# Performance work log

Hardware: AMD Instinct MI355X
Metric: run time of the kernel (lower is better)

## Reference

```python
import jax, jax.numpy as jnp
import numpy as np

N_NODES = 100000
N_EDGES = 600000
N_FEAT = 128
DIM = 128
N_LAYERS = 4
N_GRAPHS = 1000
BN_EPS = 1e-4


def setup_inputs() -> dict:
    key = jax.random.key(0)
    ks = jax.random.split(key, 12)
    s = 0.05
    x = jax.random.normal(ks[0], (N_NODES, N_FEAT), dtype=jnp.float32)
    edge_index = jax.random.randint(ks[1], (2, N_EDGES), 0, N_NODES, dtype=jnp.int64)
    batch = jnp.sort(jax.random.randint(ks[2], (N_NODES,), 0, N_GRAPHS, dtype=jnp.int64))
    pre_w = jax.random.normal(ks[3], (N_FEAT, DIM), dtype=jnp.float32) * s
    pre_b = jnp.zeros((DIM,), dtype=jnp.float32)
    # GIN MLP weights (first layer input is DIM since pre projects to DIM)
    conv_w1 = jax.random.normal(ks[4], (N_LAYERS, DIM, DIM), dtype=jnp.float32) * s
    conv_w2 = jax.random.normal(ks[5], (N_LAYERS, DIM, DIM), dtype=jnp.float32) * s
    bn_g = jnp.ones((N_LAYERS, DIM), dtype=jnp.float32)
    bn_b = jnp.zeros((N_LAYERS, DIM), dtype=jnp.float32)
    ed = DIM * N_LAYERS  # embedding_dim = 512
    ff_w1 = jax.random.normal(ks[6], (ed, ed), dtype=jnp.float32) * s
    ff_w2 = jax.random.normal(ks[7], (ed, ed), dtype=jnp.float32) * s
    ff_w3 = jax.random.normal(ks[8], (ed, ed), dtype=jnp.float32) * s
    ff_sc = jax.random.normal(ks[9], (ed, ed), dtype=jnp.float32) * s
    return dict(x=x, edge_index=edge_index, batch=batch, pre_w=pre_w, pre_b=pre_b,
                conv_w1=conv_w1, conv_w2=conv_w2, bn_g=bn_g, bn_b=bn_b,
                ff_w1=ff_w1, ff_w2=ff_w2, ff_w3=ff_w3, ff_sc=ff_sc)


def reference(x, edge_index, batch, pre_w, pre_b, conv_w1, conv_w2, bn_g, bn_b,
              ff_w1, ff_w2, ff_w3, ff_sc):
    lrelu = jax.nn.leaky_relu  # negative_slope=0.01 matches torch default
    n = x.shape[0]
    src, dst = edge_index[0], edge_index[1]

    h = x @ pre_w + pre_b  # [N, DIM]
    xs = []
    for i in range(conv_w1.shape[0]):
        # GINConv (eps=0): nn(x + sum_{j->i} x_j); gather at src, scatter-add at dst
        agg = jax.ops.segment_sum(h[src], dst, num_segments=n)
        h2 = h + agg
        h2 = lrelu(h2 @ conv_w1[i]) @ conv_w2[i]
        # BatchNorm1d (training mode, biased variance, eps=1e-4)
        mean = jnp.mean(h2, axis=0)
        var = jnp.var(h2, axis=0)
        h = (h2 - mean) * jax.lax.rsqrt(var + BN_EPS) * bn_g[i] + bn_b[i]
        xs.append(h)

    # global_add_pool per layer, then concat -> [G, DIM*L]
    pooled = [jax.ops.segment_sum(hl, batch, num_segments=N_GRAPHS) for hl in xs]
    y = jnp.concatenate(pooled, axis=1)

    z = lrelu(lrelu(lrelu(y @ ff_w1) @ ff_w2) @ ff_w3) + y @ ff_sc
    return z
```

## Files before the change

kernel.cpp:

```cpp
#include <hip/hip_runtime.h>
#include <hip/hip_bf16.h>

typedef __hip_bfloat16 bf16;
typedef unsigned int u32;
typedef __attribute__((ext_vector_type(8))) short short8v;
typedef __attribute__((ext_vector_type(4))) float f32x4;

__device__ __forceinline__ float lrelu_f(float v) { return v > 0.f ? v : 0.01f * v; }
__device__ __forceinline__ float bf_lo(u32 u) { return __uint_as_float(u << 16); }
__device__ __forceinline__ float bf_hi(u32 u) { return __uint_as_float(u & 0xffff0000u); }
__device__ __forceinline__ unsigned short bbits(float v) {
    union { bf16 b; unsigned short s; } u; u.b = __float2bfloat16(v); return u.s;
}
__device__ __forceinline__ u32 pack2(float a, float b) {
    return (u32)bbits(a) | ((u32)bbits(b) << 16);
}
__device__ __forceinline__ float ld_ext(const void* p, size_t idx, int f32f) {
    return f32f ? ((const float*)p)[idx] : __bfloat162float(((const bf16*)p)[idx]);
}

__global__ void probe_k(const int* __restrict__ ei, const int* __restrict__ batch,
                        const u32* __restrict__ bng, int nedges, int nnodes,
                        int* __restrict__ flags, float* __restrict__ scaleA,
                        float* __restrict__ shiftA)
{
    __shared__ int nz[2];
    if (threadIdx.x < 2) nz[threadIdx.x] = 0;
    __syncthreads();
    int t = threadIdx.x;
    if (ei[(nedges + 2 * t) | 1] != 0) atomicAdd(&nz[0], 1);
    if (batch[((nnodes >> 1) + 2 * t) | 1] != 0) atomicAdd(&nz[1], 1);
    if (t < 128) { scaleA[t] = 1.f; shiftA[t] = 0.f; }
    __syncthreads();
    if (t == 0) {
        flags[0] = (nz[0] == 0) ? 1 : 0;
        flags[1] = (nz[1] == 0) ? 1 : 0;
        flags[2] = (bng[0] == 0x3F800000u) ? 1 : 0;
    }
}

__global__ __launch_bounds__(256)
void hist_k(const int* __restrict__ ei, int* __restrict__ deg, int nedges,
            const int* __restrict__ flags)
{
    int e = blockIdx.x * 256 + threadIdx.x;
    if (e >= nedges) return;
    int f = flags[0];
    int dst = f ? ei[(nedges + e) << 1] : ei[nedges + e];
    atomicAdd(&deg[dst], 1);
}

__global__ __launch_bounds__(256)
void scan1_k(const int* __restrict__ deg, int* __restrict__ bsum, int n)
{
    __shared__ int l[256];
    int t = threadIdx.x, i = blockIdx.x * 256 + t;
    l[t] = (i < n) ? deg[i] : 0;
    __syncthreads();
    for (int off = 128; off > 0; off >>= 1) {
        if (t < off) l[t] += l[t + off];
        __syncthreads();
    }
    if (t == 0) bsum[blockIdx.x] = l[0];
}
__global__ __launch_bounds__(1024)
void scan2_k(int* __restrict__ bsum, int nb)
{
    __shared__ int l[1024];
    int t = threadIdx.x;
    int orig = (t < nb) ? bsum[t] : 0;
    l[t] = orig;
    __syncthreads();
    for (int off = 1; off < 1024; off <<= 1) {
        int v = (t >= off) ? l[t - off] : 0;
        __syncthreads();
        l[t] += v;
        __syncthreads();
    }
    if (t < nb) bsum[t] = l[t] - orig;
}
__global__ __launch_bounds__(256)
void scan3_k(const int* __restrict__ deg, const int* __restrict__ bsum,
             int* __restrict__ rowptr, int* __restrict__ cursor, int n)
{
    __shared__ int l[256];
    int t = threadIdx.x, i = blockIdx.x * 256 + t;
    int d = (i < n) ? deg[i] : 0;
    l[t] = d;
    __syncthreads();
    for (int off = 1; off < 256; off <<= 1) {
        int v = (t >= off) ? l[t - off] : 0;
        __syncthreads();
        l[t] += v;
        __syncthreads();
    }
    int excl = l[t] - d + bsum[blockIdx.x];
    if (i < n) {
        rowptr[i] = excl;
        cursor[i] = excl;
        if (i == n - 1) rowptr[n] = excl + d;
    }
}

__global__ __launch_bounds__(256)
void fill_k(const int* __restrict__ ei, int* __restrict__ cursor,
            int* __restrict__ srcs, int nedges, const int* __restrict__ flags)
{
    int e = blockIdx.x * 256 + threadIdx.x;
    if (e >= nedges) return;
    int f = flags[0];
    int src = ei[e << f];
    int dst = f ? ei[(nedges + e) << 1] : ei[nedges + e];
    int pos = atomicAdd(&cursor[dst], 1);
    srcs[pos] = src;
}

__global__ __launch_bounds__(256)
void wprep_all_k(const void* __restrict__ pre_w, const void* __restrict__ w1,
                 const void* __restrict__ w2, const void* __restrict__ f0,
                 const void* __restrict__ f1, const void* __restrict__ f2,
                 const void* __restrict__ f3, bf16* __restrict__ Wf,
                 const int* __restrict__ flags)
{
    int e = blockIdx.x * 256 + threadIdx.x;
    if (e >= 1196032) return;
    const void* W; int K, wstride, l, r;
    if (e < 16384)       { W = pre_w; K = 128; wstride = 128; l = 0; r = e; }
    else if (e < 81920)  { int q = e - 16384; W = w1; K = 128; wstride = 128; l = q >> 14; r = q & 16383; }
    else if (e < 147456) { int q = e - 81920; W = w2; K = 128; wstride = 128; l = q >> 14; r = q & 16383; }
    else {
        int q = e - 147456; int m = q >> 18; r = q & 262143;
        W = (m == 0) ? f0 : (m == 1) ? f1 : (m == 2) ? f2 : f3;
        K = 512; wstride = 512; l = 0;
    }
    int KS = K >> 5;
    int j = r & 7, lane = (r >> 3) & 63;
    int rem = r >> 9;
    int ks = rem % KS, nt = rem / KS;
    int k = ks * 32 + ((lane >> 4) << 3) + j;
    int n = nt * 16 + (lane & 15);
    Wf[e] = __float2bfloat16(ld_ext(W, (size_t)(l * K + k) * wstride + n, flags[2]));
}

template<int SRC, int MODE, int OBF>
__global__ __launch_bounds__(256)
void mgemm_k(const void* __restrict__ A, const bf16* __restrict__ Wf,
             const void* __restrict__ bias, void* __restrict__ out,
             int nrows, int K, int astride, int ostride, const int* __restrict__ flags)
{
    const int KS = K >> 5;
    const int t = threadIdx.x, w = t >> 6, lane = t & 63;
    const int quad = lane >> 4, lr = lane & 15;
    const int rbase = blockIdx.x * 64 + w * 16;
    const int arow = min(rbase + lr, nrows - 1);
    const int ntg0 = blockIdx.y * 8;
    const int f32f = flags[2];

    f32x4 acc[8];
    #pragma unroll
    for (int i = 0; i < 8; ++i) acc[i] = (f32x4){0.f, 0.f, 0.f, 0.f};

    for (int ks = 0; ks < KS; ++ks) {
        const int kof = ks * 32 + quad * 8;
        short8v a;
        if (SRC == 0 || f32f) {
            const float* Af = (const float*)A + (size_t)arow * astride + kof;
            float4 p0 = *(const float4*)Af;
            float4 p1 = *(const float4*)(Af + 4);
            a[0] = (short)bbits(p0.x); a[1] = (short)bbits(p0.y);
            a[2] = (short)bbits(p0.z); a[3] = (short)bbits(p0.w);
            a[4] = (short)bbits(p1.x); a[5] = (short)bbits(p1.y);
            a[6] = (short)bbits(p1.z); a[7] = (short)bbits(p1.w);
        } else {
            a = *(const short8v*)((const short*)A + (size_t)arow * astride + kof);
        }
        #pragma unroll
        for (int nt = 0; nt < 8; ++nt) {
            const short8v b = *(const short8v*)&Wf[(((size_t)(ntg0 + nt) * KS + ks) * 64 + lane) * 8];
            acc[nt] = __builtin_amdgcn_mfma_f32_16x16x32_bf16(a, b, acc[nt], 0, 0, 0);
        }
    }

    #pragma unroll
    for (int nt = 0; nt < 8; ++nt) {
        const int col = (ntg0 + nt) * 16 + lr;
        float bv = 0.f;
        if (MODE == 0 && bias != nullptr) bv = ld_ext(bias, col, f32f);
        #pragma unroll
        for (int r = 0; r < 4; ++r) {
            int orow = rbase + quad * 4 + r;
            if (orow < nrows) {
                float v = acc[nt][r] + bv;
                if (MODE == 1) v = lrelu_f(v);
                if (OBF) ((bf16*)out)[(size_t)orow * ostride + col] = __float2bfloat16(v);
                else     ((float*)out)[(size_t)orow * ostride + col] = v;
            }
        }
    }
}

__global__ __launch_bounds__(256, 2)
void conv_k(const u32* __restrict__ aggb, const bf16* __restrict__ Wf1,
            const bf16* __restrict__ Wf2, u32* __restrict__ h2,
            float* __restrict__ psum, float* __restrict__ psq,
            int nrows, int ntiles, int npairs)
{
    __shared__ bf16 PT[2][16][136];
    __shared__ float sblk[128], qblk[128];
    const int t = threadIdx.x, w = t >> 6, lane = t & 63;
    const int quad = lane >> 4, lr = lane & 15;
    const int pair = w >> 1, hw = w & 1;
    const int gpair = blockIdx.x * 2 + pair;
    const int chb = hw * 64;

    short8v w1f[4][4], w2f[4][4];
    #pragma unroll
    for (int i = 0; i < 4; ++i)
        #pragma unroll
        for (int ks = 0; ks < 4; ++ks) {
            int ntb = hw * 4 + i;
            w1f[i][ks] = *(const short8v*)&Wf1[((ntb * 4 + ks) * 64 + lane) * 8];
            w2f[i][ks] = *(const short8v*)&Wf2[((ntb * 4 + ks) * 64 + lane) * 8];
        }

    if (t < 128) { sblk[t] = 0.f; qblk[t] = 0.f; }
    __syncthreads();

    f32x4 s8[4], q8[4];
    #pragma unroll
    for (int i = 0; i < 4; ++i) { s8[i] = (f32x4){0,0,0,0}; q8[i] = (f32x4){0,0,0,0}; }

    const int iters = (ntiles + npairs - 1) / npairs;
    for (int it = 0; it < iters; ++it) {
        const int tile = gpair + it * npairs;
        const bool act = tile < ntiles;
        const int nodeu = act ? tile * 16 + lr : 0;
        const int node = min(nodeu, nrows - 1);
        const bool valid = act && (nodeu < nrows);

        if (act) {
            f32x4 acc[4];
            #pragma unroll
            for (int i = 0; i < 4; ++i) acc[i] = (f32x4){0,0,0,0};
            #pragma unroll
            for (int ks = 0; ks < 4; ++ks) {
                const short8v bfrag = *(const short8v*)&aggb[(size_t)node * 64 + ks * 16 + quad * 4];
                #pragma unroll
                for (int i = 0; i < 4; ++i)
                    acc[i] = __builtin_amdgcn_mfma_f32_16x16x32_bf16(w1f[i][ks], bfrag, acc[i], 0, 0, 0);
            }
            #pragma unroll
            for (int i = 0; i < 4; ++i) {
                u32* dp = (u32*)&PT[pair][lr][chb + i * 16 + quad * 4];
                dp[0] = pack2(lrelu_f(acc[i][0]), lrelu_f(acc[i][1]));
                dp[1] = pack2(lrelu_f(acc[i][2]), lrelu_f(acc[i][3]));
            }
        }
        __syncthreads();
        if (act) {
            f32x4 acc2[4];
            #pragma unroll
            for (int i = 0; i < 4; ++i) acc2[i] = (f32x4){0,0,0,0};
            #pragma unroll
            for (int ks = 0; ks < 4; ++ks) {
                const short8v pfrag = *(const short8v*)&PT[pair][lr][ks * 32 + quad * 8];
                #pragma unroll
                for (int i = 0; i < 4; ++i)
                    acc2[i] = __builtin_amdgcn_mfma_f32_16x16x32_bf16(w2f[i][ks], pfrag, acc2[i], 0, 0, 0);
            }
            if (valid) {
                #pragma unroll
                for (int i = 0; i < 4; ++i) {
                    u32* o = &h2[(size_t)nodeu * 64 + (chb >> 1) + i * 8 + quad * 2];
                    o[0] = pack2(acc2[i][0], acc2[i][1]);
                    o[1] = pack2(acc2[i][2], acc2[i][3]);
                    s8[i] += acc2[i];
                    q8[i] += acc2[i] * acc2[i];
                }
            }
        }
        __syncthreads();
    }

    #pragma unroll
    for (int i = 0; i < 4; ++i)
        #pragma unroll
        for (int r = 0; r < 4; ++r) {
            int ch = chb + i * 16 + quad * 4 + r;
            atomicAdd(&sblk[ch], s8[i][r]);
            atomicAdd(&qblk[ch], q8[i][r]);
        }
    __syncthreads();
    if (t < 128) {
        psum[(size_t)blockIdx.x * 128 + t] = sblk[t];
        psq[(size_t)blockIdx.x * 128 + t] = qblk[t];
    }
}

__global__ __launch_bounds__(256)
void reduce_bn_k(const float* __restrict__ psum, const float* __restrict__ psq,
                 const void* __restrict__ g, const void* __restrict__ b,
                 float* __restrict__ scale, float* __restrict__ shift,
                 float inv_n, int layer, int nblk, const int* __restrict__ flags)
{
    __shared__ float ls[256], lq[256];
    int c = blockIdx.x, t = threadIdx.x;
    float s = 0.f, q = 0.f;
    for (int i = t; i < nblk; i += 256) {
        s += psum[(size_t)i * 128 + c];
        q += psq[(size_t)i * 128 + c];
    }
    ls[t] = s; lq[t] = q;
    __syncthreads();
    for (int off = 128; off > 0; off >>= 1) {
        if (t < off) { ls[t] += ls[t + off]; lq[t] += lq[t + off]; }
        __syncthreads();
    }
    if (t == 0) {
        int f32f = flags[2];
        size_t off = (size_t)layer * 128 + c;
        float mean = ls[0] * inv_n;
        float var = lq[0] * inv_n - mean * mean;
        float sc = ld_ext(g, off, f32f) * rsqrtf(fmaxf(var, 0.f) + 1e-4f);
        scale[c] = sc;
        shift[c] = ld_ext(b, off, f32f) - mean * sc;
    }
}

__global__ __launch_bounds__(256)
void aggregate_k(const int* __restrict__ rowptr, const int* __restrict__ srcs,
                 const u32* __restrict__ h2, u32* __restrict__ aggb,
                 const float* __restrict__ scale, const float* __restrict__ shift, int nnodes)
{
    int node = blockIdx.x * 4 + (threadIdx.x >> 6);
    if (node >= nnodes) return;
    int lane = threadIdx.x & 63;
    u32 u = h2[(size_t)node * 64 + lane];
    float ax = bf_lo(u), ay = bf_hi(u);
    int lo = rowptr[node], hi = rowptr[node + 1];
    int e = lo;
    for (; e + 4 <= hi; e += 4) {
        int s0 = srcs[e], s1 = srcs[e + 1], s2 = srcs[e + 2], s3 = srcs[e + 3];
        u32 v0 = h2[(size_t)s0 * 64 + lane];
        u32 v1 = h2[(size_t)s1 * 64 + lane];
        u32 v2 = h2[(size_t)s2 * 64 + lane];
        u32 v3 = h2[(size_t)s3 * 64 + lane];
        ax += bf_lo(v0) + bf_lo(v1) + bf_lo(v2) + bf_lo(v3);
        ay += bf_hi(v0) + bf_hi(v1) + bf_hi(v2) + bf_hi(v3);
    }
    for (; e < hi; ++e) {
        u32 v = h2[(size_t)srcs[e] * 64 + lane];
        ax += bf_lo(v);
        ay += bf_hi(v);
    }
    float cnt = (float)(hi - lo + 1);
    int c = lane * 2;
    float r0 = fmaf(ax, scale[c], shift[c] * cnt);
    float r1 = fmaf(ay, scale[c + 1], shift[c + 1] * cnt);
    aggb[(size_t)node * 64 + lane] = pack2(r0, r1);
}

__device__ __forceinline__ int lower_bound_b(const int* b, int n, int key, int fb)
{
    int lo = 0, hi = n;
    while (lo < hi) {
        int m = (lo + hi) >> 1;
        if (b[m << fb] < key) lo = m + 1; else hi = m;
    }
    return lo;
}

__global__ __launch_bounds__(256)
void pool_k(const u32* __restrict__ h2, const int* __restrict__ batch,
            float* __restrict__ y, int layer, int nnodes, int ngraphs,
            const float* __restrict__ scale, const float* __restrict__ shift,
            const int* __restrict__ flags)
{
    int g = blockIdx.x * 4 + (threadIdx.x >> 6);
    if (g >= ngraphs) return;
    int t = threadIdx.x & 63;
    int fb = flags[1];
    int lo = lower_bound_b(batch, nnodes, g, fb);
    int hi = lower_bound_b(batch, nnodes, g + 1, fb);
    float s0 = 0.f, s1 = 0.f;
    int i = lo;
    for (; i + 4 <= hi; i += 4) {
        u32 u0 = h2[(size_t)i * 64 + t];
        u32 u1 = h2[(size_t)(i + 1) * 64 + t];
        u32 u2 = h2[(size_t)(i + 2) * 64 + t];
        u32 u3 = h2[(size_t)(i + 3) * 64 + t];
        s0 += bf_lo(u0) + bf_lo(u1) + bf_lo(u2) + bf_lo(u3);
        s1 += bf_hi(u0) + bf_hi(u1) + bf_hi(u2) + bf_hi(u3);
    }
    for (; i < hi; ++i) {
        u32 u = h2[(size_t)i * 64 + t];
        s0 += bf_lo(u);
        s1 += bf_hi(u);
    }
    float cnt = (float)(hi - lo);
    int c = t * 2;
    float* yp = &y[(size_t)g * 512 + layer * 128 + c];
    yp[0] = fmaf(s0, scale[c], shift[c] * cnt);
    yp[1] = fmaf(s1, scale[c + 1], shift[c + 1] * cnt);
}

__global__ __launch_bounds__(256)
void final_k(const float* __restrict__ a, const float* __restrict__ b,
             float* __restrict__ out, int n)
{
    int i = blockIdx.x * 256 + threadIdx.x;
    if (i < n) out[i] = a[i] + b[i];
}

extern "C" void kernel_launch(void* const* d_in, const int* in_sizes, int n_in,
                              void* d_out, int out_size, void* d_ws, size_t ws_size,
                              hipStream_t stream)
{
    const void* x       = d_in[0];
    const int*  ei      = (const int*)d_in[1];
    const int*  batch   = (const int*)d_in[2];
    const void* pre_w   = d_in[3];
    const void* pre_b   = d_in[4];
    const void* conv_w1 = d_in[5];
    const void* conv_w2 = d_in[6];
    const void* bn_g    = d_in[7];
    const void* bn_b    = d_in[8];

    const int n_nodes  = in_sizes[2];
    const int n_edges  = in_sizes[1] / 2;
    const int n_graphs = out_size / 512;
    const size_t nf = (size_t)n_nodes * 128;
    const int nsb = (n_nodes + 255) / 256;
    const int NCONVB = 512;
    const int ntiles = (n_nodes + 15) / 16;
    const int npairs = NCONVB * 2;

    float* ws      = (float*)d_ws;
    int*   flags   = (int*)ws;
    int*   bsum    = (int*)(ws + 16);
    float* scaleA  = ws + 1056;
    float* shiftA  = scaleA + 5 * 128;
    float* psum    = shiftA + 5 * 128;
    float* psq     = psum + (size_t)NCONVB * 128;
    float* y       = psq + (size_t)NCONVB * 128;
    float* tA      = y  + (size_t)n_graphs * 512;
    float* tB      = tA + (size_t)n_graphs * 512;
    u32*   bufA    = (u32*)(tB + (size_t)n_graphs * 512);
    u32*   bufB    = bufA + nf / 2;
    int*   deg     = (int*)(bufB + nf / 2);
    int*   rowptr  = deg + n_nodes;
    int*   srcs    = rowptr + n_nodes + 1;
    bf16*  Wfn     = (bf16*)(((uintptr_t)(srcs + n_edges) + 15) & ~(uintptr_t)15);
    bf16*  Wff     = Wfn + 9 * 16384;

    probe_k<<<1, 256, 0, stream>>>(ei, batch, (const u32*)bn_g, n_edges, n_nodes,
                                   flags, scaleA, shiftA);

    hipMemsetAsync(deg, 0, n_nodes * sizeof(int), stream);
    hist_k<<<(n_edges + 255) / 256, 256, 0, stream>>>(ei, deg, n_edges, flags);
    scan1_k<<<nsb, 256, 0, stream>>>(deg, bsum, n_nodes);
    scan2_k<<<1, 1024, 0, stream>>>(bsum, nsb);
    scan3_k<<<nsb, 256, 0, stream>>>(deg, bsum, rowptr, deg, n_nodes);
    fill_k<<<(n_edges + 255) / 256, 256, 0, stream>>>(ei, deg, srcs, n_edges, flags);

    wprep_all_k<<<(1196032 + 255) / 256, 256, 0, stream>>>(
        pre_w, conv_w1, conv_w2, d_in[9], d_in[10], d_in[11], d_in[12], Wfn, flags);

    const dim3 gpre((n_nodes + 63) / 64, 1);
    const dim3 gf((n_graphs + 63) / 64, 4);

    mgemm_k<1, 0, 1><<<gpre, 256, 0, stream>>>(x, Wfn, pre_b, bufA, n_nodes, 128, 128, 128, flags);

    for (int l = 0; l < 4; ++l) {
        aggregate_k<<<(n_nodes + 3) / 4, 256, 0, stream>>>(
            rowptr, srcs, bufA, bufB, scaleA + l * 128, shiftA + l * 128, n_nodes);
        conv_k<<<NCONVB, 256, 0, stream>>>(bufB, Wfn + (1 + l) * 16384, Wfn + (5 + l) * 16384,
                                           bufA, psum, psq, n_nodes, ntiles, npairs);
        reduce_bn_k<<<128, 256, 0, stream>>>(psum, psq, bn_g, bn_b,
                                             scaleA + (l + 1) * 128, shiftA + (l + 1) * 128,
                                             1.f / (float)n_nodes, l, NCONVB, flags);
        pool_k<<<(n_graphs + 3) / 4, 256, 0, stream>>>(
            bufA, batch, y, l, n_nodes, n_graphs,
            scaleA + (l + 1) * 128, shiftA + (l + 1) * 128, flags);
    }

    mgemm_k<0, 0, 0><<<gf, 256, 0, stream>>>(y,  Wff + 3ull * 262144, nullptr, tB, n_graphs, 512, 512, 512, flags);
    mgemm_k<0, 1, 0><<<gf, 256, 0, stream>>>(y,  Wff + 0ull * 262144, nullptr, tA, n_graphs, 512, 512, 512, flags);
    mgemm_k<0, 1, 0><<<gf, 256, 0, stream>>>(tA, Wff + 1ull * 262144, nullptr, y,  n_graphs, 512, 512, 512, flags);
    mgemm_k<0, 1, 0><<<gf, 256, 0, stream>>>(y,  Wff + 2ull * 262144, nullptr, tA, n_graphs, 512, 512, 512, flags);

    final_k<<<(n_graphs * 512 + 255) / 256, 256, 0, stream>>>(tA, tB, (float*)d_out, n_graphs * 512);
}
```

Before: 811.3 us.

## Add persistent register-weight pre-projection kernel and prefetch conv input tiles

Replaces the generic mgemm pre-projection with a persistent kernel that keeps the weight fragments in registers and converts x to bf16 on the fly. conv_k now prefetches the next tile's aggregated input while computing the current one, and uses wider vector stores. BN partial statistics are now accumulated with per-tile LDS atomics instead of register accumulators flushed once at the end. This frees registers, but the extra LDS atomics in the inner loop add contention.

Measured after the change: 1.381 ms. 1.7x slower.

```diff
diff --git a/kernel.cpp b/kernel.cpp
--- a/kernel.cpp
+++ b/kernel.cpp
@@ -200,6 +200,73 @@
 }
 
 __global__ __launch_bounds__(256, 2)
+void pre_k(const void* __restrict__ x, const bf16* __restrict__ Wf,
+           const void* __restrict__ bias, u32* __restrict__ h,
+           int nrows, int ntiles, int npairs, const int* __restrict__ flags)
+{
+    const int t = threadIdx.x, w = t >> 6, lane = t & 63;
+    const int quad = lane >> 4, lr = lane & 15;
+    const int gpair = blockIdx.x * 2 + (w >> 1);
+    const int hw = w & 1;
+    const int chb = hw * 64;
+    const int f32f = flags[2];
+
+    short8v wf[4][4];
+    #pragma unroll
+    for (int i = 0; i < 4; ++i)
+        #pragma unroll
+        for (int ks = 0; ks < 4; ++ks) {
+            wf[i][ks] = *(const short8v*)&Wf[(((hw * 4 + i) * 4 + ks) * 64 + lane) * 8];
+            asm volatile("" : "+v"(wf[i][ks]));
+        }
+    float bv[4][4];
+    #pragma unroll
+    for (int i = 0; i < 4; ++i)
+        #pragma unroll
+        for (int r = 0; r < 4; ++r)
+            bv[i][r] = ld_ext(bias, chb + i * 16 + quad * 4 + r, f32f);
+
+    const int iters = (ntiles + npairs - 1) / npairs;
+    for (int it = 0; it < iters; ++it) {
+        const int tile = gpair + it * npairs;
+        if (tile >= ntiles) break;
+        const int nodeu = tile * 16 + lr;
+        const int node = min(nodeu, nrows - 1);
+
+        f32x4 acc[4];
+        #pragma unroll
+        for (int i = 0; i < 4; ++i) acc[i] = (f32x4){0,0,0,0};
+        #pragma unroll
+        for (int ks = 0; ks < 4; ++ks) {
+            short8v bfrag;
+            if (f32f) {
+                const float* xp = (const float*)x + (size_t)node * 128 + ks * 32 + quad * 8;
+                float4 p0 = *(const float4*)xp;
+                float4 p1 = *(const float4*)(xp + 4);
+                bfrag[0] = (short)bbits(p0.x); bfrag[1] = (short)bbits(p0.y);
+                bfrag[2] = (short)bbits(p0.z); bfrag[3] = (short)bbits(p0.w);
+                bfrag[4] = (short)bbits(p1.x); bfrag[5] = (short)bbits(p1.y);
+                bfrag[6] = (short)bbits(p1.z); bfrag[7] = (short)bbits(p1.w);
+            } else {
+                bfrag = *(const short8v*)((const short*)x + (size_t)node * 128 + ks * 32 + quad * 8);
+            }
+            #pragma unroll
+            for (int i = 0; i < 4; ++i)
+                acc[i] = __builtin_amdgcn_mfma_f32_16x16x32_bf16(wf[i][ks], bfrag, acc[i], 0, 0, 0);
+        }
+        if (nodeu < nrows) {
+            #pragma unroll
+            for (int i = 0; i < 4; ++i) {
+                uint2 o;
+                o.x = pack2(acc[i][0] + bv[i][0], acc[i][1] + bv[i][1]);
+                o.y = pack2(acc[i][2] + bv[i][2], acc[i][3] + bv[i][3]);
+                *(uint2*)&h[(size_t)nodeu * 64 + (chb >> 1) + i * 8 + quad * 2] = o;
+            }
+        }
+    }
+}
+
+__global__ __launch_bounds__(256, 2)
 void conv_k(const u32* __restrict__ aggb, const bf16* __restrict__ Wf1,
             const bf16* __restrict__ Wf2, u32* __restrict__ h2,
             float* __restrict__ psum, float* __restrict__ psq,
@@ -221,43 +288,55 @@
             int ntb = hw * 4 + i;
             w1f[i][ks] = *(const short8v*)&Wf1[((ntb * 4 + ks) * 64 + lane) * 8];
             w2f[i][ks] = *(const short8v*)&Wf2[((ntb * 4 + ks) * 64 + lane) * 8];
+            asm volatile("" : "+v"(w1f[i][ks]));
+            asm volatile("" : "+v"(w2f[i][ks]));
         }
 
     if (t < 128) { sblk[t] = 0.f; qblk[t] = 0.f; }
     __syncthreads();
 
-    f32x4 s8[4], q8[4];
-    #pragma unroll
-    for (int i = 0; i < 4; ++i) { s8[i] = (f32x4){0,0,0,0}; q8[i] = (f32x4){0,0,0,0}; }
+    int tileC = gpair;
+    bool actC = tileC < ntiles;
+    int nodeuC = tileC * 16 + lr;
+    short8v bcur[4];
+    if (actC) {
+        int nd = min(nodeuC, nrows - 1);
+        #pragma unroll
+        for (int ks = 0; ks < 4; ++ks)
+            bcur[ks] = *(const short8v*)&aggb[(size_t)nd * 64 + ks * 16 + quad * 4];
+    }
 
     const int iters = (ntiles + npairs - 1) / npairs;
     for (int it = 0; it < iters; ++it) {
-        const int tile = gpair + it * npairs;
-        const bool act = tile < ntiles;
-        const int nodeu = act ? tile * 16 + lr : 0;
-        const int node = min(nodeu, nrows - 1);
-        const bool valid = act && (nodeu < nrows);
-
-        if (act) {
+        const int tileN = tileC + npairs;
+        const bool actN = tileN < ntiles;
+        short8v bnxt[4];
+        if (actN) {
+            int ndN = min(tileN * 16 + lr, nrows - 1);
+            #pragma unroll
+            for (int ks = 0; ks < 4; ++ks)
+                bnxt[ks] = *(const short8v*)&aggb[(size_t)ndN * 64 + ks * 16 + quad * 4];
+        }
+
+        if (actC) {
             f32x4 acc[4];
             #pragma unroll
             for (int i = 0; i < 4; ++i) acc[i] = (f32x4){0,0,0,0};
             #pragma unroll
-            for (int ks = 0; ks < 4; ++ks) {
-                const short8v bfrag = *(const short8v*)&aggb[(size_t)node * 64 + ks * 16 + quad * 4];
+            for (int ks = 0; ks < 4; ++ks)
                 #pragma unroll
                 for (int i = 0; i < 4; ++i)
-                    acc[i] = __builtin_amdgcn_mfma_f32_16x16x32_bf16(w1f[i][ks], bfrag, acc[i], 0, 0, 0);
+                    acc[i] = __builtin_amdgcn_mfma_f32_16x16x32_bf16(w1f[i][ks], bcur[ks], acc[i], 0, 0, 0);
+            #pragma unroll
+            for (int i = 0; i < 4; ++i) {
+                uint2 p;
+                p.x = pack2(lrelu_f(acc[i][0]), lrelu_f(acc[i][1]));
+                p.y = pack2(lrelu_f(acc[i][2]), lrelu_f(acc[i][3]));
+                *(uint2*)&PT[pair][lr][chb + i * 16 + quad * 4] = p;
             }
-            #pragma unroll
-            for (int i = 0; i < 4; ++i) {
-                u32* dp = (u32*)&PT[pair][lr][chb + i * 16 + quad * 4];
-                dp[0] = pack2(lrelu_f(acc[i][0]), lrelu_f(acc[i][1]));
-                dp[1] = pack2(lrelu_f(acc[i][2]), lrelu_f(acc[i][3]));
-            }
-        }
-        __syncthreads();
-        if (act) {
+        }
+        __syncthreads();
+        if (actC) {
             f32x4 acc2[4];
             #pragma unroll
             for (int i = 0; i < 4; ++i) acc2[i] = (f32x4){0,0,0,0};
@@ -268,29 +347,28 @@
                 for (int i = 0; i < 4; ++i)
                     acc2[i] = __builtin_amdgcn_mfma_f32_16x16x32_bf16(w2f[i][ks], pfrag, acc2[i], 0, 0, 0);
             }
-            if (valid) {
+            if (nodeuC < nrows) {
                 #pragma unroll
                 for (int i = 0; i < 4; ++i) {
-                    u32* o = &h2[(size_t)nodeu * 64 + (chb >> 1) + i * 8 + quad * 2];
-                    o[0] = pack2(acc2[i][0], acc2[i][1]);
-                    o[1] = pack2(acc2[i][2], acc2[i][3]);
-                    s8[i] += acc2[i];
-                    q8[i] += acc2[i] * acc2[i];
+                    uint2 o;
+                    o.x = pack2(acc2[i][0], acc2[i][1]);
+                    o.y = pack2(acc2[i][2], acc2[i][3]);
+                    *(uint2*)&h2[(size_t)nodeuC * 64 + (chb >> 1) + i * 8 + quad * 2] = o;
+                    #pragma unroll
+                    for (int r = 0; r < 4; ++r) {
+                        float v = acc2[i][r];
+                        atomicAdd(&sblk[chb + i * 16 + quad * 4 + r], v);
+                        atomicAdd(&qblk[chb + i * 16 + quad * 4 + r], v * v);
+                    }
                 }
             }
         }
         __syncthreads();
-    }
-
-    #pragma unroll
-    for (int i = 0; i < 4; ++i)
-        #pragma unroll
-        for (int r = 0; r < 4; ++r) {
-            int ch = chb + i * 16 + quad * 4 + r;
-            atomicAdd(&sblk[ch], s8[i][r]);
-            atomicAdd(&qblk[ch], q8[i][r]);
-        }
-    __syncthreads();
+        tileC = tileN; actC = actN; nodeuC = tileN * 16 + lr;
+        #pragma unroll
+        for (int ks = 0; ks < 4; ++ks) bcur[ks] = bnxt[ks];
+    }
+
     if (t < 128) {
         psum[(size_t)blockIdx.x * 128 + t] = sblk[t];
         psq[(size_t)blockIdx.x * 128 + t] = qblk[t];
@@ -466,10 +544,7 @@
     wprep_all_k<<<(1196032 + 255) / 256, 256, 0, stream>>>(
         pre_w, conv_w1, conv_w2, d_in[9], d_in[10], d_in[11], d_in[12], Wfn, flags);
 
-    const dim3 gpre((n_nodes + 63) / 64, 1);
-    const dim3 gf((n_graphs + 63) / 64, 4);
-
-    mgemm_k<1, 0, 1><<<gpre, 256, 0, stream>>>(x, Wfn, pre_b, bufA, n_nodes, 128, 128, 128, flags);
+    pre_k<<<NCONVB, 256, 0, stream>>>(x, Wfn, pre_b, bufA, n_nodes, ntiles, npairs, flags);
 
     for (int l = 0; l < 4; ++l) {
         aggregate_k<<<(n_nodes + 3) / 4, 256, 0, stream>>>(
@@ -484,6 +559,7 @@
             scaleA + (l + 1) * 128, shiftA + (l + 1) * 128, flags);
     }
 
+    const dim3 gf((n_graphs + 63) / 64, 4);
     mgemm_k<0, 0, 0><<<gf, 256, 0, stream>>>(y,  Wff + 3ull * 262144, nullptr, tB, n_graphs, 512, 512, 512, flags);
     mgemm_k<0, 1, 0><<<gf, 256, 0, stream>>>(y,  Wff + 0ull * 262144, nullptr, tA, n_graphs, 512, 512, 512, flags);
     mgemm_k<0, 1, 0><<<gf, 256, 0, stream>>>(tA, Wff + 1ull * 262144, nullptr, y,  n_graphs, 512, 512, 512, flags);
```
